# Kernel optimization log

Measured on AMD Instinct MI355X. Metric: run time of the kernel, lower is better.

The kernel has to match this reference:

```python
import jax, jax.numpy as jnp
import numpy as np

NUM_CLASSES = 80
NUM_KERNELS = 256
NUM_GRIDS = (40, 36, 24, 16, 12)
STRIDES = (8, 8, 16, 32, 32)
SCORE_THR = 0.1
MASK_THR = 0.5
UPDATE_THR = 0.05
NMS_PRE = 500
MAX_PER_IMG = 100
NMS_SIGMA = 2.0
ORI_H, ORI_W = 640, 960  # ratio*f_h = 4*160, 4*240 -> upsampled == ori size


def point_nms(heat, kernel=2):
    # torch: hmax = max_pool2d(heat, 2, stride=1, padding=1)[..., :-1, :-1]
    # equivalent: 2x2 window with (1,0) padding top/left, -inf init
    hmax = jax.lax.reduce_window(
        heat, -jnp.inf, jax.lax.max,
        (1, 1, kernel, kernel), (1, 1, 1, 1),
        ((0, 0), (0, 0), (1, 0), (1, 0)))
    return heat * (hmax == heat).astype(heat.dtype)


def setup_inputs() -> dict:
    key = jax.random.key(0)
    ks = jax.random.split(key, 11)
    inp = {}
    for i, g in enumerate(NUM_GRIDS):
        inp[f"cate_p{i}"] = jax.random.normal(ks[i], (1, NUM_CLASSES, g, g), jnp.float32)
        inp[f"kern_p{i}"] = jax.random.normal(ks[5 + i], (1, NUM_KERNELS, g, g), jnp.float32) * 0.05
    inp["mask_feat"] = jax.random.normal(ks[10], (1, NUM_KERNELS, 160, 240), jnp.float32)
    return inp


def _solo_post(cate_list, kern_list, mask_feat):
    # point-NMS on sigmoid scores, flatten grids, concat levels  -> [S, C]
    cate = jnp.concatenate([
        point_nms(jax.nn.sigmoid(c))[0].transpose(1, 2, 0).reshape(-1, NUM_CLASSES)
        for c in cate_list], axis=0)
    kern = jnp.concatenate([
        k[0].transpose(1, 2, 0).reshape(-1, NUM_KERNELS) for k in kern_list], axis=0)
    strides = jnp.concatenate([
        jnp.full((g * g,), float(s), jnp.float32) for g, s in zip(NUM_GRIDS, STRIDES)])

    # score threshold -> fixed-size top-k selection (jit-friendly)
    flat = jnp.where(cate > SCORE_THR, cate, 0.0).reshape(-1)  # [S*C]
    scores, flat_idx = jax.lax.top_k(flat, NMS_PRE)
    grid_idx = flat_idx // NUM_CLASSES
    labels = flat_idx % NUM_CLASSES
    valid = scores > 0.0

    # 1x1 dynamic conv == matmul over channel dim
    kp = kern[grid_idx]                                   # [N, K]
    st = strides[grid_idx]                                # [N]
    seg = jax.nn.sigmoid(jnp.einsum('nk,khw->nhw', kp, mask_feat[0]))  # [N, h, w]
    seg_masks = seg > MASK_THR
    sum_masks = seg_masks.sum((1, 2)).astype(jnp.float32)
    keep = (sum_masks > st) & valid
    seg_score = (seg * seg_masks).sum((1, 2)) / jnp.maximum(sum_masks, 1.0)
    scores = scores * seg_score * keep.astype(scores.dtype)

    # sort descending by updated scores
    order = jnp.argsort(-scores)
    scores = scores[order]
    labels = labels[order]
    seg = seg[order]
    alive = (scores > 0.0).astype(jnp.float32)
    masks_f = seg_masks[order].astype(jnp.float32) * alive[:, None, None]
    sum_m = masks_f.sum((1, 2))

    # matrix NMS (gaussian)
    mflat = masks_f.reshape(NMS_PRE, -1)
    inter = mflat @ mflat.T                               # [N, N]
    union = sum_m[:, None] + sum_m[None, :] - inter
    iou = jnp.triu(jnp.where(union > 0, inter / jnp.maximum(union, 1.0), 0.0), k=1)
    label_m = jnp.triu((labels[:, None] == labels[None, :]).astype(jnp.float32), k=1)
    decay_iou = iou * label_m
    comp_iou = decay_iou.max(axis=0)                      # per instance (column max)
    # decay[i, j] = exp(-sigma*(decay_iou[i,j]^2 - comp_iou[i]^2)); coef = min over i
    decay = jnp.exp(-NMS_SIGMA * (decay_iou ** 2 - comp_iou[:, None] ** 2))
    scores = scores * decay.min(axis=0)

    scores = scores * (scores >= UPDATE_THR).astype(scores.dtype)
    top_s, top_i = jax.lax.top_k(scores, MAX_PER_IMG)
    seg_top = seg[top_i]                                  # [M, h, w]

    # upsample to (f_h*ratio, f_w*ratio) then to ori_size (equal here), crop no-op
    up = jax.image.resize(seg_top, (MAX_PER_IMG, ORI_H, ORI_W), method='bilinear')
    up2 = jax.image.resize(up, (MAX_PER_IMG, ORI_H, ORI_W), method='bilinear')
    return up2, top_s, top_i, labels


def reference(cate_p0, cate_p1, cate_p2, cate_p3, cate_p4,
              kern_p0, kern_p1, kern_p2, kern_p3, kern_p4, mask_feat):
    up2, top_s, top_i, labels = _solo_post(
        [cate_p0, cate_p1, cate_p2, cate_p3, cate_p4],
        [kern_p0, kern_p1, kern_p2, kern_p3, kern_p4], mask_feat)
    pred_masks = up2 > MASK_THR
    return pred_masks, top_s, labels[top_i]
```

## Files before the change

kernel.cpp:

```cpp
#include <hip/hip_runtime.h>
#include <stdint.h>

#define NCLS 80
#define NKER 256
#define STOT 3872
#define NFLAT (STOT*NCLS)
#define NPRE 500
#define NPREP 512
#define MAXI 100
#define MH 160
#define MW 240
#define MP (MH*MW)
#define OH 640
#define OW 960
#define NWORD 600
#define PARTW 300

#define BN 128
#define BP 128
#define BK 16

#define WS_HIST   0u
#define WS_META   262144u
#define WS_CMP    266240u
#define WS_ZEROB  270336u
#define WS_PIOU   274432u
#define WS_FLAT   2266240u
#define WS_CANDV  3505280u
#define WS_CANDI  3521664u
#define WS_SEL    3538048u
#define WS_KPT    3591296u
#define WS_MB     4115584u
#define WS_PART   6515584u
#define WS_SEG    7715584u
#define WS_PLIST  WS_FLAT

__device__ __forceinline__ float bf2f(unsigned short u) { return __uint_as_float(((unsigned)u) << 16); }
__device__ __forceinline__ unsigned short f2bf(float f) {
  unsigned b = __float_as_uint(f);
  return (unsigned short)((b + 0x7fffu + ((b >> 16) & 1u)) >> 16);
}
__device__ __forceinline__ unsigned fkey(float f) {
  unsigned b = __float_as_uint(f);
  return b ^ ((b & 0x80000000u) ? 0xFFFFFFFFu : 0x80000000u);
}

__global__ __launch_bounds__(256) void k_flat(
    const float* __restrict__ c0, const float* __restrict__ c1, const float* __restrict__ c2,
    const float* __restrict__ c3, const float* __restrict__ c4,
    float* __restrict__ flat, unsigned* __restrict__ hist) {
  int idx = blockIdx.x * 256 + threadIdx.x;
  if (idx >= NFLAT) return;
  int s = idx / NCLS, c = idx - s * NCLS;
  const float* base; int g, cell;
  if (s < 1600)      { base = c0; g = 40; cell = s; }
  else if (s < 2896) { base = c1; g = 36; cell = s - 1600; }
  else if (s < 3472) { base = c2; g = 24; cell = s - 2896; }
  else if (s < 3728) { base = c3; g = 16; cell = s - 3472; }
  else               { base = c4; g = 12; cell = s - 3728; }
  int i = cell / g, j = cell - i * g;
  const float* ch = base + c * g * g;
  float x = ch[i * g + j];
  float m = x;
  if (i > 0 && j > 0) m = fmaxf(m, ch[(i - 1) * g + j - 1]);
  if (i > 0)          m = fmaxf(m, ch[(i - 1) * g + j]);
  if (j > 0)          m = fmaxf(m, ch[i * g + j - 1]);
  bool pass = (x >= m) && ((double)x > -2.1972245773362196 );
  flat[idx] = pass ? x : __int_as_float(0xFF800000);
  if (pass) atomicAdd(&hist[fkey(x) >> 16], 1u);
}

__global__ void k_pivot(const unsigned* __restrict__ hist, unsigned* __restrict__ meta) {
  __shared__ unsigned csum[1024];
  int t = threadIdx.x;
  int hi = 65536 - t * 64, lo = hi - 64;
  unsigned s = 0;
  for (int b = lo; b < hi; ++b) s += hist[b];
  csum[t] = s;
  __syncthreads();
  if (t == 0) {
    unsigned cum = 0;
    for (int cch = 0; cch < 1024; ++cch) {
      if (cum + csum[cch] >= NPRE) {
        int chi = 65536 - cch * 64;
        for (int b = chi - 1; b >= chi - 64; --b) {
          if (cum + hist[b] >= NPRE) { meta[1] = (unsigned)b; return; }
          cum += hist[b];
        }
      }
      cum += csum[cch];
    }
    meta[1] = 0u;
  }
}

__global__ __launch_bounds__(256) void k_compact(
    const float* __restrict__ flat, float* __restrict__ cv, int* __restrict__ ci,
    unsigned* __restrict__ meta) {
  int idx = blockIdx.x * 256 + threadIdx.x;
  if (idx >= NFLAT) return;
  float v = flat[idx];
  if (__float_as_uint(v) == 0xFF800000u) return;
  if ((fkey(v) >> 16) >= meta[1]) {
    unsigned pos = atomicAdd(&meta[0], 1u);
    if (pos < 4096u) { cv[pos] = v; ci[pos] = idx; }
  }
}

__global__ __launch_bounds__(1024) void k_select(
    const float* __restrict__ cv, const int* __restrict__ ci, const unsigned* __restrict__ meta,
    double* __restrict__ sel_score, unsigned* __restrict__ sel_grid,
    unsigned* __restrict__ sel_label, double* __restrict__ sel_stride) {
  __shared__ float sv[4096];
  __shared__ int si[4096];
  int t = threadIdx.x;
  int n = (meta[0] < 4096u) ? (int)meta[0] : 4096;
  for (int i = t; i < 4096; i += 1024) {
    if (i < n) { sv[i] = cv[i]; si[i] = ci[i]; }
    else       { sv[i] = __int_as_float(0xFF800000); si[i] = (1 << 30) + i; }
  }
  __syncthreads();
  for (int k = 2; k <= 4096; k <<= 1)
    for (int j = k >> 1; j > 0; j >>= 1) {
      for (int i = t; i < 4096; i += 1024) {
        int ix = i ^ j;
        if (ix > i) {
          float v1 = sv[i], v2 = sv[ix]; int i1 = si[i], i2 = si[ix];
          bool b2 = (v2 > v1) || (v2 == v1 && i2 < i1);
          bool dir = (i & k) == 0;
          if (dir == b2) { sv[i] = v2; sv[ix] = v1; si[i] = i2; si[ix] = i1; }
        }
      }
      __syncthreads();
    }
  for (int i = t; i < NPREP; i += 1024) {
    if (i < NPRE && i < n) {
      int fidx = si[i];
      unsigned gi = (unsigned)fidx / NCLS;
      sel_score[i] = 1.0 / (1.0 + exp(-(double)sv[i]));
      sel_grid[i] = gi;
      sel_label[i] = (unsigned)fidx - gi * NCLS;
      sel_stride[i] = gi < 2896u ? 8.0 : (gi < 3472u ? 16.0 : 32.0);
    } else {
      sel_score[i] = 0.0; sel_grid[i] = 0u; sel_label[i] = 0u; sel_stride[i] = 1e18;
    }
  }
}

__global__ __launch_bounds__(256) void k_gather(
    const float* __restrict__ k0, const float* __restrict__ k1, const float* __restrict__ k2,
    const float* __restrict__ k3, const float* __restrict__ k4,
    const unsigned* __restrict__ sel_grid, float* __restrict__ kpT) {
  int tid = blockIdx.x * 256 + threadIdx.x;
  if (tid >= NPREP * NKER) return;
  int n = tid & (NPREP - 1);
  int k = tid >> 9;
  float v = 0.f;
  if (n < NPRE) {
    unsigned gi = sel_grid[n];
    const float* base; unsigned g, cell;
    if (gi < 1600u)      { base = k0; g = 40; cell = gi; }
    else if (gi < 2896u) { base = k1; g = 36; cell = gi - 1600u; }
    else if (gi < 3472u) { base = k2; g = 24; cell = gi - 2896u; }
    else if (gi < 3728u) { base = k3; g = 16; cell = gi - 3472u; }
    else                 { base = k4; g = 12; cell = gi - 3728u; }
    v = base[(unsigned)k * g * g + cell];
  }
  kpT[k * NPREP + n] = v;
}

__global__ __launch_bounds__(256, 2) void k_gemm(
    const float* __restrict__ kpT, const float* __restrict__ mf,
    unsigned short* __restrict__ seg, unsigned long long* __restrict__ mb,
    double* __restrict__ part) {
  __shared__ double Asd[BK][BN];
  __shared__ double Bsd[BK][BP];
  int p0 = blockIdx.x * BP, n0 = blockIdx.y * BN;
  int tid = threadIdx.x;
  int tp = tid & 15, tn = tid >> 4;
  double acc[8][8] = {};
  float2 ra[4], rb[4];
#pragma unroll
  for (int it = 0; it < 4; ++it) {
    int q = it * 256 + tid; int row = q >> 6, c2 = q & 63;
    ra[it] = *(const float2*)&kpT[row * NPREP + n0 + c2 * 2];
    rb[it] = *(const float2*)&mf[(size_t)row * MP + p0 + c2 * 2];
  }
  for (int kc = 0; kc < NKER; kc += BK) {
#pragma unroll
    for (int it = 0; it < 4; ++it) {
      int q = it * 256 + tid; int row = q >> 6, c2 = q & 63;
      double2 da; da.x = (double)ra[it].x; da.y = (double)ra[it].y;
      double2 db; db.x = (double)rb[it].x; db.y = (double)rb[it].y;
      *(double2*)&Asd[row][c2 * 2] = da;
      *(double2*)&Bsd[row][c2 * 2] = db;
    }
    __syncthreads();
    if (kc + BK < NKER) {
#pragma unroll
      for (int it = 0; it < 4; ++it) {
        int q = it * 256 + tid; int row = q >> 6, c2 = q & 63;
        ra[it] = *(const float2*)&kpT[(kc + BK + row) * NPREP + n0 + c2 * 2];
        rb[it] = *(const float2*)&mf[(size_t)(kc + BK + row) * MP + p0 + c2 * 2];
      }
    }
#pragma unroll 4
    for (int k = 0; k < BK; ++k) {
      double2 A0 = *(double2*)&Asd[k][tn * 8 + 0];
      double2 A1 = *(double2*)&Asd[k][tn * 8 + 2];
      double2 A2 = *(double2*)&Asd[k][tn * 8 + 4];
      double2 A3 = *(double2*)&Asd[k][tn * 8 + 6];
      double2 B0 = *(double2*)&Bsd[k][tp * 2];
      double2 B1 = *(double2*)&Bsd[k][32 + tp * 2];
      double2 B2 = *(double2*)&Bsd[k][64 + tp * 2];
      double2 B3 = *(double2*)&Bsd[k][96 + tp * 2];
      double a[8] = {A0.x, A0.y, A1.x, A1.y, A2.x, A2.y, A3.x, A3.y};
      double b[8] = {B0.x, B0.y, B1.x, B1.y, B2.x, B2.y, B3.x, B3.y};
#pragma unroll
      for (int r = 0; r < 8; ++r)
#pragma unroll
        for (int c = 0; c < 8; ++c)
          acc[r][c] = fma(a[r], b[c], acc[r][c]);
    }
    __syncthreads();
  }
  double* partL = (double*)&Asd[0][0];
  unsigned* nibL = (unsigned*)&Bsd[0][0];
  for (int r = 0; r < 8; ++r) {
    int nl = (tn << 3) + r;
    int nn = n0 + nl;
    unsigned nb = 0; double wsum = 0.0;
    unsigned short u[8];
#pragma unroll
    for (int c = 0; c < 8; ++c) {
      float z = (float)acc[r][c];
      float sf = 1.0f / (1.0f + __expf(-z));
      u[c] = f2bf(sf);
      if (acc[r][c] > 0.0) { nb |= 1u << c; wsum += (double)sf; }
    }
    if (nn < NPRE) {
#pragma unroll
      for (int g = 0; g < 4; ++g) {
        ushort2 o; o.x = u[2 * g]; o.y = u[2 * g + 1];
        *(ushort2*)&seg[(size_t)nn * MP + p0 + g * 32 + tp * 2] = o;
      }
    }
    partL[nl * 16 + tp] = wsum;
    nibL[nl * 16 + tp] = nb;
  }
  __syncthreads();
  if (tid < 128) {
    int nn = n0 + tid;
    if (nn < NPRE) {
      double ssum = 0.0; unsigned long long w0 = 0ull, w1 = 0ull;
#pragma unroll
      for (int c = 0; c < 16; ++c) {
        ssum += partL[tid * 16 + c];
        unsigned long long nb = (unsigned long long)nibL[tid * 16 + c];
        w0 |= ((nb      & 3ull) << (c * 2)) | (((nb >> 2) & 3ull) << (32 + c * 2));
        w1 |= (((nb >> 4) & 3ull) << (c * 2)) | (((nb >> 6) & 3ull) << (32 + c * 2));
      }
      int bx = blockIdx.x;
      part[nn * PARTW + bx] = ssum;
      mb[nn * NWORD + bx * 2] = w0;
      mb[nn * NWORD + bx * 2 + 1] = w1;
    }
  }
}

__global__ void k_masks(const unsigned long long* __restrict__ mb, const double* __restrict__ part,
                        const double* __restrict__ sel_score, const double* __restrict__ sel_stride,
                        double* __restrict__ summask, double* __restrict__ upd) {
  int n = blockIdx.x, t = threadIdx.x;
  int cnt = 0; double ws = 0.0;
  for (int j = t; j < NWORD; j += 64) cnt += __popcll(mb[n * NWORD + j]);
  for (int j = t; j < PARTW; j += 64) ws += part[n * PARTW + j];
  for (int o = 32; o > 0; o >>= 1) { cnt += __shfl_down(cnt, o); ws += __shfl_down(ws, o); }
  if (t == 0) {
    double cf = (double)cnt;
    double ss = ws / fmax(cf, 1.0);
    double raw = sel_score[n];
    bool keep = (cf > sel_stride[n]) && (raw > 0.0);
    summask[n] = cf;
    upd[n] = keep ? raw * ss : 0.0;
  }
}

__global__ __launch_bounds__(512) void k_sort(
    const double* __restrict__ upd, const unsigned* __restrict__ sel_label, const double* __restrict__ summask,
    double* __restrict__ s_score, unsigned* __restrict__ s_slot, unsigned* __restrict__ s_label2,
    double* __restrict__ s_sum, unsigned* __restrict__ plist, unsigned* __restrict__ meta) {
  __shared__ double sv[NPREP];
  __shared__ int si[NPREP];
  __shared__ unsigned labv[NPREP];
  int t = threadIdx.x;
  sv[t] = (t < NPRE) ? upd[t] : -1.0;
  si[t] = t;
  __syncthreads();
  for (int k = 2; k <= NPREP; k <<= 1)
    for (int j = k >> 1; j > 0; j >>= 1) {
      int ix = t ^ j;
      if (ix > t) {
        double v1 = sv[t], v2 = sv[ix]; int i1 = si[t], i2 = si[ix];
        bool b2 = (v2 > v1) || (v2 == v1 && i2 < i1);
        bool dir = (t & k) == 0;
        if (dir == b2) { sv[t] = v2; sv[ix] = v1; si[t] = i2; si[ix] = i1; }
      }
      __syncthreads();
    }
  double sc = sv[t]; int slot = si[t];
  bool alive = sc > 0.0;
  unsigned lab = sel_label[slot];
  s_score[t] = alive ? sc : 0.0;
  s_slot[t] = (unsigned)slot;
  s_label2[t] = lab;
  s_sum[t] = (alive && slot < NPRE) ? summask[slot] : 0.0;
  labv[t] = alive ? lab : (0x10000u + (unsigned)t);
  __syncthreads();
  if (t < NPRE) {
    unsigned li = labv[t];
    if (li < 0x10000u) {
      for (int j = t + 1; j < NPRE; ++j) {
        if (labv[j] == li) {
          unsigned pos = atomicAdd(&meta[2], 1u);
          plist[pos] = ((unsigned)t << 16) | (unsigned)j;
        }
      }
    }
  }
}

__global__ __launch_bounds__(256) void k_inter(
    const unsigned long long* __restrict__ mb, const unsigned* __restrict__ s_slot,
    const double* __restrict__ s_sum, const unsigned* __restrict__ plist,
    const unsigned* __restrict__ meta, double* __restrict__ piou,
    unsigned long long* __restrict__ cmp_bits) {
  int wid = (blockIdx.x * 256 + threadIdx.x) >> 6;
  int lane = threadIdx.x & 63;
  unsigned npair = meta[2];
  for (unsigned pp = wid; pp < npair; pp += 256) {
    unsigned pk = plist[pp];
    int i = (int)(pk >> 16), j = (int)(pk & 0xFFFFu);
    const unsigned long long* A = mb + (size_t)s_slot[i] * NWORD;
    const unsigned long long* B = mb + (size_t)s_slot[j] * NWORD;
    int c = 0;
    for (int wd = lane; wd < NWORD; wd += 64) c += __popcll(A[wd] & B[wd]);
    for (int o = 32; o > 0; o >>= 1) c += __shfl_down(c, o);
    if (lane == 0) {
      double inter = (double)c;
      double uni = s_sum[i] + s_sum[j] - inter;
      double val = (uni > 0.0) ? inter / fmax(uni, 1.0) : 0.0;
      piou[pp] = val;
      if (val > 0.0)
        atomicMax(&cmp_bits[j], (unsigned long long)__double_as_longlong(val));
    }
  }
}

__global__ __launch_bounds__(512) void k_top(
    const unsigned* __restrict__ plist, const unsigned* __restrict__ meta,
    const double* __restrict__ piou, const unsigned long long* __restrict__ cmp_bits,
    const double* __restrict__ s_score, const unsigned* __restrict__ s_label2,
    const unsigned* __restrict__ s_slot,
    float* __restrict__ d_out, int maskN, unsigned* __restrict__ up_slot) {
  __shared__ unsigned long long mS[NPREP];
  __shared__ double sv[NPREP];
  __shared__ int si[NPREP];
  int t = threadIdx.x;
  mS[t] = 0ull;
  __syncthreads();
  unsigned npair = meta[2];
  for (unsigned p = t; p < npair; p += NPREP) {
    unsigned pk = plist[p];
    int i = (int)(pk >> 16), j = (int)(pk & 0xFFFFu);
    double d = piou[p];
    double ci = __longlong_as_double((long long)cmp_bits[i]);
    double v = d * d - ci * ci;
    if (v > 0.0)
      atomicMax(&mS[j], (unsigned long long)__double_as_longlong(v));
  }
  __syncthreads();
  double f = 0.0;
  if (t < NPRE) {
    double m = __longlong_as_double((long long)mS[t]);
    f = s_score[t] * exp(-2.0 * m);
    if (f < 0.05) f = 0.0;
  }
  sv[t] = f; si[t] = t;
  __syncthreads();
  for (int k = 2; k <= NPREP; k <<= 1)
    for (int j = k >> 1; j > 0; j >>= 1) {
      int ix = t ^ j;
      if (ix > t) {
        double v1 = sv[t], v2 = sv[ix]; int i1 = si[t], i2 = si[ix];
        bool b2 = (v2 > v1) || (v2 == v1 && i2 < i1);
        bool dir = (t & k) == 0;
        if (dir == b2) { sv[t] = v2; sv[ix] = v1; si[t] = i2; si[ix] = i1; }
      }
      __syncthreads();
    }
  if (t < MAXI) {
    int pos = si[t];
    d_out[maskN + t] = (float)sv[t];
    d_out[maskN + MAXI + t] = (float)s_label2[pos];
    up_slot[t] = s_slot[pos];
  }
}

__global__ __launch_bounds__(256) void k_up(const unsigned short* __restrict__ seg,
                                            const unsigned* __restrict__ up_slot,
                                            float* __restrict__ out, int maskN) {
  int o4 = (blockIdx.x * 256 + threadIdx.x) * 4;
  if (o4 >= maskN) return;
  int m = o4 / (OH * OW);
  int rem = o4 - m * (OH * OW);
  int y = rem / OW;
  int x = rem - y * OW;
  int a = x >> 2;
  const unsigned short* row = seg + (size_t)up_slot[m] * MP;
  float sy = y * 0.25f - 0.375f;
  int y0 = (int)floorf(sy);
  float wy = sy - y0;
  int y0c = max(y0, 0), y1c = min(y0 + 1, MH - 1);
  const unsigned short* r0 = row + y0c * MW;
  const unsigned short* r1 = row + y1c * MW;
  int t0 = max(a - 1, 0), t1 = a, t2 = min(a + 1, MW - 1);
  float T0 = bf2f(r0[t0]), T1 = bf2f(r0[t1]), T2 = bf2f(r0[t2]);
  float B0 = bf2f(r1[t0]), B1 = bf2f(r1[t1]), B2 = bf2f(r1[t2]);
  float iwy = 1.f - wy;
  float4 o;
  o.x = iwy * (0.375f * T0 + 0.625f * T1) + wy * (0.375f * B0 + 0.625f * B1);
  o.y = iwy * (0.125f * T0 + 0.875f * T1) + wy * (0.125f * B0 + 0.875f * B1);
  o.z = iwy * (0.875f * T1 + 0.125f * T2) + wy * (0.875f * B1 + 0.125f * B2);
  o.w = iwy * (0.625f * T1 + 0.375f * T2) + wy * (0.625f * B1 + 0.375f * B2);
  o.x = (o.x > 0.5f) ? 1.f : 0.f;
  o.y = (o.y > 0.5f) ? 1.f : 0.f;
  o.z = (o.z > 0.5f) ? 1.f : 0.f;
  o.w = (o.w > 0.5f) ? 1.f : 0.f;
  *(float4*)&out[o4] = o;
}

extern "C" void kernel_launch(void* const* d_in, const int* in_sizes, int n_in,
                              void* d_out, int out_size, void* d_ws, size_t ws_size,
                              hipStream_t stream) {
  const float* c0 = (const float*)d_in[0];
  const float* k0 = (const float*)d_in[1];
  const float* c1 = (const float*)d_in[2];
  const float* k1 = (const float*)d_in[3];
  const float* c2 = (const float*)d_in[4];
  const float* k2 = (const float*)d_in[5];
  const float* c3 = (const float*)d_in[6];
  const float* k3 = (const float*)d_in[7];
  const float* c4 = (const float*)d_in[8];
  const float* k4 = (const float*)d_in[9];
  const float* mf = (const float*)d_in[10];

  char* ws = (char*)d_ws;
  unsigned* hist = (unsigned*)(ws + WS_HIST);
  unsigned* meta = (unsigned*)(ws + WS_META);
  unsigned long long* cmp_bits = (unsigned long long*)(ws + WS_CMP);
  double* piou = (double*)(ws + WS_PIOU);
  float* flat = (float*)(ws + WS_FLAT);
  float* cv = (float*)(ws + WS_CANDV);
  int* ci = (int*)(ws + WS_CANDI);
  double* sel_score  = (double*)(ws + WS_SEL + 0);
  unsigned* sel_grid = (unsigned*)(ws + WS_SEL + 4096);
  unsigned* sel_label= (unsigned*)(ws + WS_SEL + 8192);
  double* sel_stride = (double*)(ws + WS_SEL + 12288);
  double* upd        = (double*)(ws + WS_SEL + 16384);
  double* summask    = (double*)(ws + WS_SEL + 20480);
  double* s_score    = (double*)(ws + WS_SEL + 24576);
  unsigned* s_slot   = (unsigned*)(ws + WS_SEL + 28672);
  unsigned* s_label2 = (unsigned*)(ws + WS_SEL + 32768);
  double* s_sum      = (double*)(ws + WS_SEL + 36864);
  unsigned* up_slot  = (unsigned*)(ws + WS_SEL + 49152);
  float* kpT = (float*)(ws + WS_KPT);
  unsigned long long* mb = (unsigned long long*)(ws + WS_MB);
  double* part = (double*)(ws + WS_PART);
  unsigned short* seg = (unsigned short*)(ws + WS_SEG);
  unsigned* plist = (unsigned*)(ws + WS_PLIST);

  int maskN = out_size - 2 * MAXI;

  hipMemsetAsync(ws, 0, WS_ZEROB, stream);

  k_flat<<<(NFLAT + 255) / 256, 256, 0, stream>>>(c0, c1, c2, c3, c4, flat, hist);
  k_pivot<<<1, 1024, 0, stream>>>(hist, meta);
  k_compact<<<(NFLAT + 255) / 256, 256, 0, stream>>>(flat, cv, ci, meta);
  k_select<<<1, 1024, 0, stream>>>(cv, ci, meta, sel_score, sel_grid, sel_label, sel_stride);
  k_gather<<<(NPREP * NKER + 255) / 256, 256, 0, stream>>>(k0, k1, k2, k3, k4, sel_grid, kpT);
  dim3 g6(MP / BP, NPREP / BN);
  k_gemm<<<g6, 256, 0, stream>>>(kpT, mf, seg, mb, part);
  k_masks<<<NPRE, 64, 0, stream>>>(mb, part, sel_score, sel_stride, summask, upd);
  k_sort<<<1, NPREP, 0, stream>>>(upd, sel_label, summask, s_score, s_slot, s_label2, s_sum, plist, meta);
  k_inter<<<64, 256, 0, stream>>>(mb, s_slot, s_sum, plist, meta, piou, cmp_bits);
  k_top<<<1, NPREP, 0, stream>>>(plist, meta, piou, cmp_bits, s_score, s_label2, s_slot,
                                 (float*)d_out, maskN, up_slot);
  k_up<<<(maskN / 4 + 255) / 256, 256, 0, stream>>>(seg, up_slot, (float*)d_out, maskN);
}
```

Before: 592.6 us.

## Fuse selection and post-processing kernels into single-block kernels

Merges pivot search, candidate compaction and bitonic selection into one single-block kernel that scans the flat score buffer itself, using shared-memory counters. Mask stats, score sort, pairwise IoU and matrix-NMS top-k are merged into one 512-thread block with shared-memory state in place of global workspace arrays. This cuts several kernel launches and global round-trips, but the compaction scan over ~310K elements and the pairwise IoU now each run on a single workgroup instead of a full grid.

```diff
diff --git a/kernel.cpp b/kernel.cpp
--- a/kernel.cpp
+++ b/kernel.cpp
@@ -21,13 +21,9 @@
 #define BK 16
 
 #define WS_HIST   0u
-#define WS_META   262144u
-#define WS_CMP    266240u
-#define WS_ZEROB  270336u
+#define WS_ZEROB  262144u
 #define WS_PIOU   274432u
 #define WS_FLAT   2266240u
-#define WS_CANDV  3505280u
-#define WS_CANDI  3521664u
 #define WS_SEL    3538048u
 #define WS_KPT    3591296u
 #define WS_MB     4115584u
@@ -70,55 +66,52 @@
   if (pass) atomicAdd(&hist[fkey(x) >> 16], 1u);
 }
 
-__global__ void k_pivot(const unsigned* __restrict__ hist, unsigned* __restrict__ meta) {
-  __shared__ unsigned csum[1024];
-  int t = threadIdx.x;
-  int hi = 65536 - t * 64, lo = hi - 64;
-  unsigned s = 0;
-  for (int b = lo; b < hi; ++b) s += hist[b];
-  csum[t] = s;
-  __syncthreads();
-  if (t == 0) {
-    unsigned cum = 0;
-    for (int cch = 0; cch < 1024; ++cch) {
-      if (cum + csum[cch] >= NPRE) {
-        int chi = 65536 - cch * 64;
-        for (int b = chi - 1; b >= chi - 64; --b) {
-          if (cum + hist[b] >= NPRE) { meta[1] = (unsigned)b; return; }
-          cum += hist[b];
-        }
-      }
-      cum += csum[cch];
-    }
-    meta[1] = 0u;
-  }
-}
-
-__global__ __launch_bounds__(256) void k_compact(
-    const float* __restrict__ flat, float* __restrict__ cv, int* __restrict__ ci,
-    unsigned* __restrict__ meta) {
-  int idx = blockIdx.x * 256 + threadIdx.x;
-  if (idx >= NFLAT) return;
-  float v = flat[idx];
-  if (__float_as_uint(v) == 0xFF800000u) return;
-  if ((fkey(v) >> 16) >= meta[1]) {
-    unsigned pos = atomicAdd(&meta[0], 1u);
-    if (pos < 4096u) { cv[pos] = v; ci[pos] = idx; }
-  }
-}
-
-__global__ __launch_bounds__(1024) void k_select(
-    const float* __restrict__ cv, const int* __restrict__ ci, const unsigned* __restrict__ meta,
+__global__ __launch_bounds__(1024) void k_sel(
+    const float* __restrict__ flat, const unsigned* __restrict__ hist,
     double* __restrict__ sel_score, unsigned* __restrict__ sel_grid,
     unsigned* __restrict__ sel_label, double* __restrict__ sel_stride) {
   __shared__ float sv[4096];
   __shared__ int si[4096];
+  __shared__ unsigned csum[1024];
+  __shared__ unsigned pivotS, cntS;
   int t = threadIdx.x;
-  int n = (meta[0] < 4096u) ? (int)meta[0] : 4096;
-  for (int i = t; i < 4096; i += 1024) {
-    if (i < n) { sv[i] = cv[i]; si[i] = ci[i]; }
-    else       { sv[i] = __int_as_float(0xFF800000); si[i] = (1 << 30) + i; }
-  }
+  if (t == 0) cntS = 0u;
+  {
+    int hi = 65536 - t * 64, lo = hi - 64;
+    unsigned s = 0;
+    for (int b = lo; b < hi; ++b) s += hist[b];
+    csum[t] = s;
+  }
+  __syncthreads();
+  if (t == 0) {
+    unsigned cum = 0, piv = 0u; bool found = false;
+    for (int cch = 0; cch < 1024 && !found; ++cch) {
+      if (cum + csum[cch] >= NPRE) {
+        int chi = 65536 - cch * 64;
+        for (int b = chi - 1; b >= chi - 64; --b) {
+          if (cum + hist[b] >= NPRE) { piv = (unsigned)b; found = true; break; }
+          cum += hist[b];
+        }
+      } else {
+        cum += csum[cch];
+      }
+    }
+    pivotS = piv;
+  }
+  __syncthreads();
+  unsigned piv = pivotS;
+  for (int idx = t; idx < NFLAT; idx += 1024) {
+    float v = flat[idx];
+    if (__float_as_uint(v) == 0xFF800000u) continue;
+    if ((fkey(v) >> 16) >= piv) {
+      unsigned pos = atomicAdd(&cntS, 1u);
+      if (pos < 4096u) { sv[pos] = v; si[pos] = idx; }
+    }
+  }
+  __syncthreads();
+  int n = (cntS < 4096u) ? (int)cntS : 4096;
+  for (int i = t; i < 4096; i += 1024)
+    if (i >= n) { sv[i] = __int_as_float(0xFF800000); si[i] = (1 << 30) + i; }
   __syncthreads();
   for (int k = 2; k <= 4096; k <<= 1)
     for (int j = k >> 1; j > 0; j >>= 1) {
@@ -268,33 +261,45 @@
   }
 }
 
-__global__ void k_masks(const unsigned long long* __restrict__ mb, const double* __restrict__ part,
-                        const double* __restrict__ sel_score, const double* __restrict__ sel_stride,
-                        double* __restrict__ summask, double* __restrict__ upd) {
-  int n = blockIdx.x, t = threadIdx.x;
-  int cnt = 0; double ws = 0.0;
-  for (int j = t; j < NWORD; j += 64) cnt += __popcll(mb[n * NWORD + j]);
-  for (int j = t; j < PARTW; j += 64) ws += part[n * PARTW + j];
-  for (int o = 32; o > 0; o >>= 1) { cnt += __shfl_down(cnt, o); ws += __shfl_down(ws, o); }
-  if (t == 0) {
-    double cf = (double)cnt;
-    double ss = ws / fmax(cf, 1.0);
-    double raw = sel_score[n];
-    bool keep = (cf > sel_stride[n]) && (raw > 0.0);
-    summask[n] = cf;
-    upd[n] = keep ? raw * ss : 0.0;
-  }
-}
-
-__global__ __launch_bounds__(512) void k_sort(
-    const double* __restrict__ upd, const unsigned* __restrict__ sel_label, const double* __restrict__ summask,
-    double* __restrict__ s_score, unsigned* __restrict__ s_slot, unsigned* __restrict__ s_label2,
-    double* __restrict__ s_sum, unsigned* __restrict__ plist, unsigned* __restrict__ meta) {
+__global__ __launch_bounds__(512) void k_post(
+    const unsigned long long* __restrict__ mb, const double* __restrict__ part,
+    const double* __restrict__ sel_score, const double* __restrict__ sel_stride,
+    const unsigned* __restrict__ sel_label,
+    unsigned* __restrict__ plist, double* __restrict__ piou,
+    float* __restrict__ d_out, int maskN, unsigned* __restrict__ up_slot) {
+  __shared__ double updL[NPREP];
+  __shared__ double summaskL[NPREP];
   __shared__ double sv[NPREP];
   __shared__ int si[NPREP];
   __shared__ unsigned labv[NPREP];
+  __shared__ double s_scoreL[NPREP];
+  __shared__ unsigned s_slotL[NPREP];
+  __shared__ unsigned s_labelL[NPREP];
+  __shared__ double s_sumL[NPREP];
+  __shared__ unsigned long long cmpL[NPREP];
+  __shared__ unsigned long long mSL[NPREP];
+  __shared__ unsigned npairS;
   int t = threadIdx.x;
-  sv[t] = (t < NPRE) ? upd[t] : -1.0;
+  int lane = t & 63, wave = t >> 6;
+  if (t == 0) npairS = 0u;
+  cmpL[t] = 0ull; mSL[t] = 0ull;
+  if (t >= NPRE) { summaskL[t] = 0.0; updL[t] = 0.0; }
+  for (int nn = wave; nn < NPRE; nn += 8) {
+    int cnt = 0; double ws = 0.0;
+    for (int j = lane; j < NWORD; j += 64) cnt += __popcll(mb[nn * NWORD + j]);
+    for (int j = lane; j < PARTW; j += 64) ws += part[nn * PARTW + j];
+    for (int o = 32; o > 0; o >>= 1) { cnt += __shfl_down(cnt, o); ws += __shfl_down(ws, o); }
+    if (lane == 0) {
+      double cf = (double)cnt;
+      double ss = ws / fmax(cf, 1.0);
+      double raw = sel_score[nn];
+      bool keep = (cf > sel_stride[nn]) && (raw > 0.0);
+      summaskL[nn] = cf;
+      updL[nn] = keep ? raw * ss : 0.0;
+    }
+  }
+  __syncthreads();
+  sv[t] = (t < NPRE) ? updL[t] : -1.0;
   si[t] = t;
   __syncthreads();
   for (int k = 2; k <= NPREP; k <<= 1)
@@ -308,82 +313,62 @@
       }
       __syncthreads();
     }
-  double sc = sv[t]; int slot = si[t];
-  bool alive = sc > 0.0;
-  unsigned lab = sel_label[slot];
-  s_score[t] = alive ? sc : 0.0;
-  s_slot[t] = (unsigned)slot;
-  s_label2[t] = lab;
-  s_sum[t] = (alive && slot < NPRE) ? summask[slot] : 0.0;
-  labv[t] = alive ? lab : (0x10000u + (unsigned)t);
+  {
+    double sc = sv[t]; int slot = si[t];
+    bool alive = sc > 0.0;
+    unsigned lab = sel_label[slot];
+    s_scoreL[t] = alive ? sc : 0.0;
+    s_slotL[t] = (unsigned)slot;
+    s_labelL[t] = lab;
+    s_sumL[t] = (alive && slot < NPRE) ? summaskL[slot] : 0.0;
+    labv[t] = alive ? lab : (0x10000u + (unsigned)t);
+  }
   __syncthreads();
   if (t < NPRE) {
     unsigned li = labv[t];
     if (li < 0x10000u) {
       for (int j = t + 1; j < NPRE; ++j) {
         if (labv[j] == li) {
-          unsigned pos = atomicAdd(&meta[2], 1u);
+          unsigned pos = atomicAdd(&npairS, 1u);
           plist[pos] = ((unsigned)t << 16) | (unsigned)j;
         }
       }
     }
   }
-}
-
-__global__ __launch_bounds__(256) void k_inter(
-    const unsigned long long* __restrict__ mb, const unsigned* __restrict__ s_slot,
-    const double* __restrict__ s_sum, const unsigned* __restrict__ plist,
-    const unsigned* __restrict__ meta, double* __restrict__ piou,
-    unsigned long long* __restrict__ cmp_bits) {
-  int wid = (blockIdx.x * 256 + threadIdx.x) >> 6;
-  int lane = threadIdx.x & 63;
-  unsigned npair = meta[2];
-  for (unsigned pp = wid; pp < npair; pp += 256) {
+  __syncthreads();
+  unsigned npair = npairS;
+  for (unsigned pp = wave; pp < npair; pp += 8) {
     unsigned pk = plist[pp];
     int i = (int)(pk >> 16), j = (int)(pk & 0xFFFFu);
-    const unsigned long long* A = mb + (size_t)s_slot[i] * NWORD;
-    const unsigned long long* B = mb + (size_t)s_slot[j] * NWORD;
+    const unsigned long long* A = mb + (size_t)s_slotL[i] * NWORD;
+    const unsigned long long* B = mb + (size_t)s_slotL[j] * NWORD;
     int c = 0;
     for (int wd = lane; wd < NWORD; wd += 64) c += __popcll(A[wd] & B[wd]);
     for (int o = 32; o > 0; o >>= 1) c += __shfl_down(c, o);
     if (lane == 0) {
       double inter = (double)c;
-      double uni = s_sum[i] + s_sum[j] - inter;
+      double uni = s_sumL[i] + s_sumL[j] - inter;
       double val = (uni > 0.0) ? inter / fmax(uni, 1.0) : 0.0;
       piou[pp] = val;
       if (val > 0.0)
-        atomicMax(&cmp_bits[j], (unsigned long long)__double_as_longlong(val));
-    }
-  }
-}
-
-__global__ __launch_bounds__(512) void k_top(
-    const unsigned* __restrict__ plist, const unsigned* __restrict__ meta,
-    const double* __restrict__ piou, const unsigned long long* __restrict__ cmp_bits,
-    const double* __restrict__ s_score, const unsigned* __restrict__ s_label2,
-    const unsigned* __restrict__ s_slot,
-    float* __restrict__ d_out, int maskN, unsigned* __restrict__ up_slot) {
-  __shared__ unsigned long long mS[NPREP];
-  __shared__ double sv[NPREP];
-  __shared__ int si[NPREP];
-  int t = threadIdx.x;
-  mS[t] = 0ull;
-  __syncthreads();
-  unsigned npair = meta[2];
-  for (unsigned p = t; p < npair; p += NPREP) {
+        atomicMax(&cmpL[j], (unsigned long long)__double_as_longlong(val));
+    }
+  }
+  __syncthreads();
+  for (unsigned p = t; p < npair; p += 512) {
     unsigned pk = plist[p];
     int i = (int)(pk >> 16), j = (int)(pk & 0xFFFFu);
     double d = piou[p];
-    double ci = __longlong_as_double((long long)cmp_bits[i]);
+    double ci = __longlong_as_double((long long)cmpL[i]);
     double v = d * d - ci * ci;
     if (v > 0.0)
-      atomicMax(&mS[j], (unsigned long long)__double_as_longlong(v));
+      atomicMax(&mSL[j], (unsigned long long)__double_as_longlong(v));
   }
   __syncthreads();
   double f = 0.0;
   if (t < NPRE) {
-    double m = __longlong_as_double((long long)mS[t]);
-    f = s_score[t] * exp(-2.0 * m);
+    double m = __longlong_as_double((long long)mSL[t]);
+    f = s_scoreL[t] * exp(-2.0 * m);
     if (f < 0.05) f = 0.0;
   }
   sv[t] = f; si[t] = t;
@@ -402,8 +387,8 @@
   if (t < MAXI) {
     int pos = si[t];
     d_out[maskN + t] = (float)sv[t];
-    d_out[maskN + MAXI + t] = (float)s_label2[pos];
-    up_slot[t] = s_slot[pos];
+    d_out[maskN + MAXI + t] = (float)s_labelL[pos];
+    up_slot[t] = s_slotL[pos];
   }
 }
 
@@ -457,22 +442,12 @@
 
   char* ws = (char*)d_ws;
   unsigned* hist = (unsigned*)(ws + WS_HIST);
-  unsigned* meta = (unsigned*)(ws + WS_META);
-  unsigned long long* cmp_bits = (unsigned long long*)(ws + WS_CMP);
   double* piou = (double*)(ws + WS_PIOU);
   float* flat = (float*)(ws + WS_FLAT);
-  float* cv = (float*)(ws + WS_CANDV);
-  int* ci = (int*)(ws + WS_CANDI);
   double* sel_score  = (double*)(ws + WS_SEL + 0);
   unsigned* sel_grid = (unsigned*)(ws + WS_SEL + 4096);
   unsigned* sel_label= (unsigned*)(ws + WS_SEL + 8192);
   double* sel_stride = (double*)(ws + WS_SEL + 12288);
-  double* upd        = (double*)(ws + WS_SEL + 16384);
-  double* summask    = (double*)(ws + WS_SEL + 20480);
-  double* s_score    = (double*)(ws + WS_SEL + 24576);
-  unsigned* s_slot   = (unsigned*)(ws + WS_SEL + 28672);
-  unsigned* s_label2 = (unsigned*)(ws + WS_SEL + 32768);
-  double* s_sum      = (double*)(ws + WS_SEL + 36864);
   unsigned* up_slot  = (unsigned*)(ws + WS_SEL + 49152);
   float* kpT = (float*)(ws + WS_KPT);
   unsigned long long* mb = (unsigned long long*)(ws + WS_MB);
@@ -485,16 +460,11 @@
   hipMemsetAsync(ws, 0, WS_ZEROB, stream);
 
   k_flat<<<(NFLAT + 255) / 256, 256, 0, stream>>>(c0, c1, c2, c3, c4, flat, hist);
-  k_pivot<<<1, 1024, 0, stream>>>(hist, meta);
-  k_compact<<<(NFLAT + 255) / 256, 256, 0, stream>>>(flat, cv, ci, meta);
-  k_select<<<1, 1024, 0, stream>>>(cv, ci, meta, sel_score, sel_grid, sel_label, sel_stride);
+  k_sel<<<1, 1024, 0, stream>>>(flat, hist, sel_score, sel_grid, sel_label, sel_stride);
   k_gather<<<(NPREP * NKER + 255) / 256, 256, 0, stream>>>(k0, k1, k2, k3, k4, sel_grid, kpT);
   dim3 g6(MP / BP, NPREP / BN);
   k_gemm<<<g6, 256, 0, stream>>>(kpT, mf, seg, mb, part);
-  k_masks<<<NPRE, 64, 0, stream>>>(mb, part, sel_score, sel_stride, summask, upd);
-  k_sort<<<1, NPREP, 0, stream>>>(upd, sel_label, summask, s_score, s_slot, s_label2, s_sum, plist, meta);
-  k_inter<<<64, 256, 0, stream>>>(mb, s_slot, s_sum, plist, meta, piou, cmp_bits);
-  k_top<<<1, NPREP, 0, stream>>>(plist, meta, piou, cmp_bits, s_score, s_label2, s_slot,
-                                 (float*)d_out, maskN, up_slot);
+  k_post<<<1, NPREP, 0, stream>>>(mb, part, sel_score, sel_stride, sel_label,
+                                  plist, piou, (float*)d_out, maskN, up_slot);
   k_up<<<(maskN / 4 + 255) / 256, 256, 0, stream>>>(seg, up_slot, (float*)d_out, maskN);
 }
```

After: 1.262 ms. 2.13x slower.

## Compute mask GEMM in fp32 with fp64 patch for near-zero logits; fuse selection kernels

Applied to the files above, without the earlier changes.

The mask GEMM now accumulates in fp32 instead of fp64, which halves shared-memory traffic and uses the faster FP32 FMA path. Logits whose magnitude falls below a small tolerance are logged to a list, and a new patch kernel recomputes them in fp64 to fix the mask bits and the sigmoid sums, so the thresholded masks keep fp64 fidelity. Separately, the pivot, compact and select kernels are merged into one single-block kernel, which removes two launches but makes one block scan the whole flat array. The fixed list capacity risks missing corrections if many logits sit near zero.

```diff
diff --git a/kernel.cpp b/kernel.cpp
--- a/kernel.cpp
+++ b/kernel.cpp
@@ -15,6 +15,8 @@
 #define OW 960
 #define NWORD 600
 #define PARTW 300
+#define UCAP 32768
+#define TAU 5e-4f
 
 #define BN 128
 #define BP 128
@@ -23,16 +25,17 @@
 #define WS_HIST   0u
 #define WS_META   262144u
 #define WS_CMP    266240u
-#define WS_ZEROB  270336u
+#define WS_CORR   270336u
+#define WS_ZEROB  274432u
 #define WS_PIOU   274432u
 #define WS_FLAT   2266240u
-#define WS_CANDV  3505280u
-#define WS_CANDI  3521664u
 #define WS_SEL    3538048u
 #define WS_KPT    3591296u
 #define WS_MB     4115584u
 #define WS_PART   6515584u
 #define WS_SEG    7715584u
+#define WS_ULIST  46115584u
+#define WS_UZ     46246656u
 #define WS_PLIST  WS_FLAT
 
 __device__ __forceinline__ float bf2f(unsigned short u) { return __uint_as_float(((unsigned)u) << 16); }
@@ -70,55 +73,52 @@
   if (pass) atomicAdd(&hist[fkey(x) >> 16], 1u);
 }
 
-__global__ void k_pivot(const unsigned* __restrict__ hist, unsigned* __restrict__ meta) {
-  __shared__ unsigned csum[1024];
-  int t = threadIdx.x;
-  int hi = 65536 - t * 64, lo = hi - 64;
-  unsigned s = 0;
-  for (int b = lo; b < hi; ++b) s += hist[b];
-  csum[t] = s;
-  __syncthreads();
-  if (t == 0) {
-    unsigned cum = 0;
-    for (int cch = 0; cch < 1024; ++cch) {
-      if (cum + csum[cch] >= NPRE) {
-        int chi = 65536 - cch * 64;
-        for (int b = chi - 1; b >= chi - 64; --b) {
-          if (cum + hist[b] >= NPRE) { meta[1] = (unsigned)b; return; }
-          cum += hist[b];
-        }
-      }
-      cum += csum[cch];
-    }
-    meta[1] = 0u;
-  }
-}
-
-__global__ __launch_bounds__(256) void k_compact(
-    const float* __restrict__ flat, float* __restrict__ cv, int* __restrict__ ci,
-    unsigned* __restrict__ meta) {
-  int idx = blockIdx.x * 256 + threadIdx.x;
-  if (idx >= NFLAT) return;
-  float v = flat[idx];
-  if (__float_as_uint(v) == 0xFF800000u) return;
-  if ((fkey(v) >> 16) >= meta[1]) {
-    unsigned pos = atomicAdd(&meta[0], 1u);
-    if (pos < 4096u) { cv[pos] = v; ci[pos] = idx; }
-  }
-}
-
-__global__ __launch_bounds__(1024) void k_select(
-    const float* __restrict__ cv, const int* __restrict__ ci, const unsigned* __restrict__ meta,
+__global__ __launch_bounds__(1024) void k_sel(
+    const float* __restrict__ flat, const unsigned* __restrict__ hist,
     double* __restrict__ sel_score, unsigned* __restrict__ sel_grid,
     unsigned* __restrict__ sel_label, double* __restrict__ sel_stride) {
   __shared__ float sv[4096];
   __shared__ int si[4096];
+  __shared__ unsigned csum[1024];
+  __shared__ unsigned pivotS, cntS;
   int t = threadIdx.x;
-  int n = (meta[0] < 4096u) ? (int)meta[0] : 4096;
-  for (int i = t; i < 4096; i += 1024) {
-    if (i < n) { sv[i] = cv[i]; si[i] = ci[i]; }
-    else       { sv[i] = __int_as_float(0xFF800000); si[i] = (1 << 30) + i; }
-  }
+  if (t == 0) cntS = 0u;
+  {
+    int hi = 65536 - t * 64, lo = hi - 64;
+    unsigned s = 0;
+    for (int b = lo; b < hi; ++b) s += hist[b];
+    csum[t] = s;
+  }
+  __syncthreads();
+  if (t == 0) {
+    unsigned cum = 0, piv = 0u; bool found = false;
+    for (int cch = 0; cch < 1024 && !found; ++cch) {
+      if (cum + csum[cch] >= NPRE) {
+        int chi = 65536 - cch * 64;
+        for (int b = chi - 1; b >= chi - 64; --b) {
+          if (cum + hist[b] >= NPRE) { piv = (unsigned)b; found = true; break; }
+          cum += hist[b];
+        }
+      } else {
+        cum += csum[cch];
+      }
+    }
+    pivotS = piv;
+  }
+  __syncthreads();
+  unsigned piv = pivotS;
+  for (int idx = t; idx < NFLAT; idx += 1024) {
+    float v = flat[idx];
+    if (__float_as_uint(v) == 0xFF800000u) continue;
+    if ((fkey(v) >> 16) >= piv) {
+      unsigned pos = atomicAdd(&cntS, 1u);
+      if (pos < 4096u) { sv[pos] = v; si[pos] = idx; }
+    }
+  }
+  __syncthreads();
+  int n = (cntS < 4096u) ? (int)cntS : 4096;
+  for (int i = t; i < 4096; i += 1024)
+    if (i >= n) { sv[i] = __int_as_float(0xFF800000); si[i] = (1 << 30) + i; }
   __syncthreads();
   for (int k = 2; k <= 4096; k <<= 1)
     for (int j = k >> 1; j > 0; j >>= 1) {
@@ -169,16 +169,17 @@
   kpT[k * NPREP + n] = v;
 }
 
-__global__ __launch_bounds__(256, 2) void k_gemm(
+__global__ __launch_bounds__(256, 3) void k_gemm(
     const float* __restrict__ kpT, const float* __restrict__ mf,
     unsigned short* __restrict__ seg, unsigned long long* __restrict__ mb,
-    double* __restrict__ part) {
-  __shared__ double Asd[BK][BN];
-  __shared__ double Bsd[BK][BP];
+    double* __restrict__ part, unsigned* __restrict__ ulist, float* __restrict__ uz,
+    unsigned* __restrict__ meta) {
+  __shared__ float Asf[BK][BN];
+  __shared__ float Bsf[BK][BP];
   int p0 = blockIdx.x * BP, n0 = blockIdx.y * BN;
   int tid = threadIdx.x;
   int tp = tid & 15, tn = tid >> 4;
-  double acc[8][8] = {};
+  float acc[8][8] = {};
   float2 ra[4], rb[4];
 #pragma unroll
   for (int it = 0; it < 4; ++it) {
@@ -190,10 +191,8 @@
 #pragma unroll
     for (int it = 0; it < 4; ++it) {
       int q = it * 256 + tid; int row = q >> 6, c2 = q & 63;
-      double2 da; da.x = (double)ra[it].x; da.y = (double)ra[it].y;
-      double2 db; db.x = (double)rb[it].x; db.y = (double)rb[it].y;
-      *(double2*)&Asd[row][c2 * 2] = da;
-      *(double2*)&Bsd[row][c2 * 2] = db;
+      *(float2*)&Asf[row][c2 * 2] = ra[it];
+      *(float2*)&Bsf[row][c2 * 2] = rb[it];
     }
     __syncthreads();
     if (kc + BK < NKER) {
@@ -206,26 +205,24 @@
     }
 #pragma unroll 4
     for (int k = 0; k < BK; ++k) {
-      double2 A0 = *(double2*)&Asd[k][tn * 8 + 0];
-      double2 A1 = *(double2*)&Asd[k][tn * 8 + 2];
-      double2 A2 = *(double2*)&Asd[k][tn * 8 + 4];
-      double2 A3 = *(double2*)&Asd[k][tn * 8 + 6];
-      double2 B0 = *(double2*)&Bsd[k][tp * 2];
-      double2 B1 = *(double2*)&Bsd[k][32 + tp * 2];
-      double2 B2 = *(double2*)&Bsd[k][64 + tp * 2];
-      double2 B3 = *(double2*)&Bsd[k][96 + tp * 2];
-      double a[8] = {A0.x, A0.y, A1.x, A1.y, A2.x, A2.y, A3.x, A3.y};
-      double b[8] = {B0.x, B0.y, B1.x, B1.y, B2.x, B2.y, B3.x, B3.y};
+      float4 A0 = *(float4*)&Asf[k][tn * 8 + 0];
+      float4 A1 = *(float4*)&Asf[k][tn * 8 + 4];
+      float2 B0 = *(float2*)&Bsf[k][tp * 2];
+      float2 B1 = *(float2*)&Bsf[k][32 + tp * 2];
+      float2 B2 = *(float2*)&Bsf[k][64 + tp * 2];
+      float2 B3 = *(float2*)&Bsf[k][96 + tp * 2];
+      float a[8] = {A0.x, A0.y, A0.z, A0.w, A1.x, A1.y, A1.z, A1.w};
+      float b[8] = {B0.x, B0.y, B1.x, B1.y, B2.x, B2.y, B3.x, B3.y};
 #pragma unroll
       for (int r = 0; r < 8; ++r)
 #pragma unroll
         for (int c = 0; c < 8; ++c)
-          acc[r][c] = fma(a[r], b[c], acc[r][c]);
+          acc[r][c] = fmaf(a[r], b[c], acc[r][c]);
     }
     __syncthreads();
   }
-  double* partL = (double*)&Asd[0][0];
-  unsigned* nibL = (unsigned*)&Bsd[0][0];
+  double* partL = (double*)&Asf[0][0];
+  __shared__ unsigned nibL[128][16];
   for (int r = 0; r < 8; ++r) {
     int nl = (tn << 3) + r;
     int nn = n0 + nl;
@@ -233,10 +230,19 @@
     unsigned short u[8];
 #pragma unroll
     for (int c = 0; c < 8; ++c) {
-      float z = (float)acc[r][c];
+      float z = acc[r][c];
       float sf = 1.0f / (1.0f + __expf(-z));
       u[c] = f2bf(sf);
-      if (acc[r][c] > 0.0) { nb |= 1u << c; wsum += (double)sf; }
+      if (z > 0.0f) { nb |= 1u << c; wsum += (double)sf; }
+      if (nn < NPRE && fabsf(z) < TAU) {
+        unsigned pos = atomicAdd(&meta[3], 1u);
+        if (pos < UCAP) {
+          int g = c >> 1, bb = c & 1;
+          int p = p0 + g * 32 + tp * 2 + bb;
+          ulist[pos] = ((unsigned)nn << 16) | (unsigned)p;
+          uz[pos] = z;
+        }
+      }
     }
     if (nn < NPRE) {
 #pragma unroll
@@ -246,7 +252,7 @@
       }
     }
     partL[nl * 16 + tp] = wsum;
-    nibL[nl * 16 + tp] = nb;
+    nibL[nl][tp] = nb;
   }
   __syncthreads();
   if (tid < 128) {
@@ -256,7 +262,7 @@
 #pragma unroll
       for (int c = 0; c < 16; ++c) {
         ssum += partL[tid * 16 + c];
-        unsigned long long nb = (unsigned long long)nibL[tid * 16 + c];
+        unsigned long long nb = (unsigned long long)nibL[tid][c];
         w0 |= ((nb      & 3ull) << (c * 2)) | (((nb >> 2) & 3ull) << (32 + c * 2));
         w1 |= (((nb >> 4) & 3ull) << (c * 2)) | (((nb >> 6) & 3ull) << (32 + c * 2));
       }
@@ -268,7 +274,39 @@
   }
 }
 
+__global__ __launch_bounds__(256) void k_patch(
+    const float* __restrict__ kpT, const float* __restrict__ mf,
+    const unsigned* __restrict__ ulist, const float* __restrict__ uz,
+    const unsigned* __restrict__ meta,
+    unsigned long long* __restrict__ mb, double* __restrict__ corr) {
+  unsigned cnt = meta[3]; if (cnt > UCAP) cnt = UCAP;
+  int wid = (blockIdx.x * 256 + threadIdx.x) >> 6;
+  int lane = threadIdx.x & 63;
+  for (unsigned e = wid; e < cnt; e += 256) {
+    unsigned pk = ulist[e];
+    int n = (int)(pk >> 16), p = (int)(pk & 0xFFFFu);
+    double d = 0.0;
+#pragma unroll
+    for (int i = 0; i < 4; ++i) {
+      int k = lane + 64 * i;
+      d = fma((double)kpT[k * NPREP + n], (double)mf[(size_t)k * MP + p], d);
+    }
+    for (int o = 32; o > 0; o >>= 1) d += __shfl_down(d, o);
+    if (lane == 0) {
+      float z32 = uz[e];
+      bool b32 = z32 > 0.0f;
+      bool b64 = d > 0.0;
+      if (b32 != b64) {
+        atomicXor(&mb[(size_t)n * NWORD + (p >> 6)], 1ull << (p & 63));
+        float sf = 1.0f / (1.0f + __expf(-z32));
+        atomicAdd(&corr[n], b64 ? (double)sf : -(double)sf);
+      }
+    }
+  }
+}
+
 __global__ void k_masks(const unsigned long long* __restrict__ mb, const double* __restrict__ part,
+                        const double* __restrict__ corr,
                         const double* __restrict__ sel_score, const double* __restrict__ sel_stride,
                         double* __restrict__ summask, double* __restrict__ upd) {
   int n = blockIdx.x, t = threadIdx.x;
@@ -277,6 +315,7 @@
   for (int j = t; j < PARTW; j += 64) ws += part[n * PARTW + j];
   for (int o = 32; o > 0; o >>= 1) { cnt += __shfl_down(cnt, o); ws += __shfl_down(ws, o); }
   if (t == 0) {
+    ws += corr[n];
     double cf = (double)cnt;
     double ss = ws / fmax(cf, 1.0);
     double raw = sel_score[n];
@@ -459,10 +498,9 @@
   unsigned* hist = (unsigned*)(ws + WS_HIST);
   unsigned* meta = (unsigned*)(ws + WS_META);
   unsigned long long* cmp_bits = (unsigned long long*)(ws + WS_CMP);
+  double* corr = (double*)(ws + WS_CORR);
   double* piou = (double*)(ws + WS_PIOU);
   float* flat = (float*)(ws + WS_FLAT);
-  float* cv = (float*)(ws + WS_CANDV);
-  int* ci = (int*)(ws + WS_CANDI);
   double* sel_score  = (double*)(ws + WS_SEL + 0);
   unsigned* sel_grid = (unsigned*)(ws + WS_SEL + 4096);
   unsigned* sel_label= (unsigned*)(ws + WS_SEL + 8192);
@@ -479,19 +517,20 @@
   double* part = (double*)(ws + WS_PART);
   unsigned short* seg = (unsigned short*)(ws + WS_SEG);
   unsigned* plist = (unsigned*)(ws + WS_PLIST);
+  unsigned* ulist = (unsigned*)(ws + WS_ULIST);
+  float* uzp = (float*)(ws + WS_UZ);
 
   int maskN = out_size - 2 * MAXI;
 
   hipMemsetAsync(ws, 0, WS_ZEROB, stream);
 
   k_flat<<<(NFLAT + 255) / 256, 256, 0, stream>>>(c0, c1, c2, c3, c4, flat, hist);
-  k_pivot<<<1, 1024, 0, stream>>>(hist, meta);
-  k_compact<<<(NFLAT + 255) / 256, 256, 0, stream>>>(flat, cv, ci, meta);
-  k_select<<<1, 1024, 0, stream>>>(cv, ci, meta, sel_score, sel_grid, sel_label, sel_stride);
+  k_sel<<<1, 1024, 0, stream>>>(flat, hist, sel_score, sel_grid, sel_label, sel_stride);
   k_gather<<<(NPREP * NKER + 255) / 256, 256, 0, stream>>>(k0, k1, k2, k3, k4, sel_grid, kpT);
   dim3 g6(MP / BP, NPREP / BN);
-  k_gemm<<<g6, 256, 0, stream>>>(kpT, mf, seg, mb, part);
-  k_masks<<<NPRE, 64, 0, stream>>>(mb, part, sel_score, sel_stride, summask, upd);
+  k_gemm<<<g6, 256, 0, stream>>>(kpT, mf, seg, mb, part, ulist, uzp, meta);
+  k_patch<<<64, 256, 0, stream>>>(kpT, mf, ulist, uzp, meta, mb, corr);
+  k_masks<<<NPRE, 64, 0, stream>>>(mb, part, corr, sel_score, sel_stride, summask, upd);
   k_sort<<<1, NPREP, 0, stream>>>(upd, sel_label, summask, s_score, s_slot, s_label2, s_sum, plist, meta);
   k_inter<<<64, 256, 0, stream>>>(mb, s_slot, s_sum, plist, meta, piou, cmp_bits);
   k_top<<<1, NPREP, 0, stream>>>(plist, meta, piou, cmp_bits, s_score, s_label2, s_slot,
```

New measurement: 976.0 us. 1.65x slower.
